# Performance work log

Hardware: AMD Instinct MI355X
Metric: run time of the kernel (lower is better)

Reference implementation:

```python
import jax, jax.numpy as jnp
import numpy as np

H2 = 512  # 2 * hidden_dim
B, TK = 64, 2048


def setup_inputs() -> dict:
    key = jax.random.key(0)
    ks = jax.random.split(key, 10)
    s_t_hat = jax.random.normal(ks[0], (B, H2), dtype=jnp.float32)
    encoder_outputs = jax.random.normal(ks[1], (B, TK, H2), dtype=jnp.float32)
    encoder_feature = jax.random.normal(ks[2], (B, TK, H2), dtype=jnp.float32)
    enc_padding_mask = jnp.ones((B, TK), dtype=jnp.float32)
    coverage = jax.random.uniform(ks[3], (B, TK), dtype=jnp.float32)
    # learned params (torch Linear stores W as [out, in]; we keep math explicit)
    sc = 1.0 / np.sqrt(H2)
    W_dp = jax.random.uniform(ks[4], (H2, H2), minval=-sc, maxval=sc, dtype=jnp.float32)  # decode_proj weight [out,in]
    b_dp = jax.random.uniform(ks[5], (H2,), minval=-sc, maxval=sc, dtype=jnp.float32)
    W_c = jax.random.uniform(ks[6], (H2,), minval=-1.0, maxval=1.0, dtype=jnp.float32)  # Linear(1, 2H) weight, squeezed
    v_w = jax.random.uniform(ks[7], (H2,), minval=-sc, maxval=sc, dtype=jnp.float32)  # Linear(2H, 1) weight
    v_b = jax.random.uniform(ks[8], (), minval=-sc, maxval=sc, dtype=jnp.float32)
    return {
        "s_t_hat": s_t_hat,
        "encoder_outputs": encoder_outputs,
        "encoder_feature": encoder_feature,
        "enc_padding_mask": enc_padding_mask,
        "coverage": coverage,
        "W_dp": W_dp,
        "b_dp": b_dp,
        "W_c": W_c,
        "v_w": v_w,
        "v_b": v_b,
    }


def reference(s_t_hat, encoder_outputs, encoder_feature, enc_padding_mask, coverage,
              W_dp, b_dp, W_c, v_w, v_b):
    # decoder projection: [b, n]
    dec_fea = s_t_hat @ W_dp.T + b_dp
    # broadcast add over t_k, plus coverage feature (Linear(1, 2H) == outer product)
    att_features = encoder_feature + dec_fea[:, None, :] + coverage[:, :, None] * W_c  # [b, t_k, n]
    e = jnp.tanh(att_features)
    scores = jnp.einsum('btn,n->bt', e, v_w) + v_b  # [b, t_k]
    attn_ = jax.nn.softmax(scores, axis=1) * enc_padding_mask
    attn = attn_ / jnp.sum(attn_, axis=1, keepdims=True)  # renormalized [b, t_k]
    c_t = jnp.einsum('bt,btn->bn', attn, encoder_outputs)  # [b, n]
    coverage_new = coverage + attn
    return (c_t, attn, coverage_new)
```

## Files before the change

### kernel.cpp

```cpp
#include <hip/hip_runtime.h>
#include <math.h>

#define H2 512
#define NB 64
#define TK 2048
#define SPLIT 16

#define LOG2E 1.44269504088896f
#define TWO_LOG2E 2.88539008177793f

__global__ __launch_bounds__(256) void k_decproj(const float* __restrict__ s,
                                                 const float* __restrict__ W,
                                                 const float* __restrict__ bias,
                                                 float* __restrict__ dec) {
    const int bb = blockIdx.x;
    const int wave = threadIdx.x >> 6;
    const int lane = threadIdx.x & 63;
    const float* srow = s + bb * H2;
    float4 s0 = *(const float4*)(srow + lane * 8);
    float4 s1 = *(const float4*)(srow + lane * 8 + 4);
    #pragma unroll
    for (int i = 0; i < 8; ++i) {
        const int n = blockIdx.y * 32 + wave * 8 + i;
        const float* wrow = W + (size_t)n * H2;
        float4 w0 = *(const float4*)(wrow + lane * 8);
        float4 w1 = *(const float4*)(wrow + lane * 8 + 4);
        float acc = s0.x * w0.x + s0.y * w0.y + s0.z * w0.z + s0.w * w0.w +
                    s1.x * w1.x + s1.y * w1.y + s1.z * w1.z + s1.w * w1.w;
        #pragma unroll
        for (int off = 1; off < 64; off <<= 1) acc += __shfl_xor(acc, off, 64);
        if (lane == 0) dec[bb * H2 + n] = acc + bias[n];
    }
}

template <int REP>
__global__ __launch_bounds__(256) void k_scores2(const float* __restrict__ ef,
                                                 const float* __restrict__ cov,
                                                 const float* __restrict__ mask,
                                                 const float* __restrict__ dec,
                                                 const float* __restrict__ wc,
                                                 const float* __restrict__ vw,
                                                 const float* __restrict__ vbp,
                                                 float* __restrict__ w) {
    const int bb = blockIdx.y;
    const int t0 = blockIdx.x * 64;
    const int tid = threadIdx.x;
    const int wave = tid >> 6, lane = tid & 63;
    const int n0 = lane * 8;

    __shared__ float pl[64][68];

    float4 d0 = *(const float4*)(dec + bb * H2 + n0);
    float4 d1 = *(const float4*)(dec + bb * H2 + n0 + 4);
    float4 c0 = *(const float4*)(wc + n0);
    float4 c1 = *(const float4*)(wc + n0 + 4);
    float4 v0 = *(const float4*)(vw + n0);
    float4 v1 = *(const float4*)(vw + n0 + 4);

    float vwsum = v0.x + v0.y + v0.z + v0.w + v1.x + v1.y + v1.z + v1.w;
    #pragma unroll
    for (int off = 1; off < 64; off <<= 1) vwsum += __shfl_xor(vwsum, off, 64);

    d0.x *= TWO_LOG2E; d0.y *= TWO_LOG2E; d0.z *= TWO_LOG2E; d0.w *= TWO_LOG2E;
    d1.x *= TWO_LOG2E; d1.y *= TWO_LOG2E; d1.z *= TWO_LOG2E; d1.w *= TWO_LOG2E;
    c0.x *= TWO_LOG2E; c0.y *= TWO_LOG2E; c0.z *= TWO_LOG2E; c0.w *= TWO_LOG2E;
    c1.x *= TWO_LOG2E; c1.y *= TWO_LOG2E; c1.z *= TWO_LOG2E; c1.w *= TWO_LOG2E;
    v0.x *= -2.f; v0.y *= -2.f; v0.z *= -2.f; v0.w *= -2.f;
    v1.x *= -2.f; v1.y *= -2.f; v1.z *= -2.f; v1.w *= -2.f;
    const float vb = vbp[0];

    const size_t rowbase = (size_t)bb * TK + t0;

    #pragma unroll 1
    for (int rep = 0; rep < REP; ++rep) {
        float4 ea[2][4][2];
        float cv[2][4];
        #pragma unroll
        for (int i = 0; i < 4; ++i) {
            const int r = wave + 4 * i;
            const float* p = ef + (rowbase + r) * H2 + n0;
            ea[0][i][0] = *(const float4*)p;
            ea[0][i][1] = *(const float4*)(p + 4);
            cv[0][i] = cov[rowbase + r];
        }
        #pragma unroll
        for (int j0 = 0; j0 < 16; j0 += 4) {
            const int cur = (j0 >> 2) & 1;
            const int nxt = cur ^ 1;
            if (j0 + 4 < 16) {
                #pragma unroll
                for (int i = 0; i < 4; ++i) {
                    const int r = wave + 4 * (j0 + 4 + i);
                    const float* p = ef + (rowbase + r) * H2 + n0;
                    ea[nxt][i][0] = *(const float4*)p;
                    ea[nxt][i][1] = *(const float4*)(p + 4);
                    cv[nxt][i] = cov[rowbase + r];
                }
            }
            #pragma unroll
            for (int i = 0; i < 4; ++i) {
                const float cvv = cv[cur][i];
                #define TERM(E, D, C, V) \
                    ((V) * __builtin_amdgcn_rcpf(__builtin_amdgcn_exp2f(fmaf((E), TWO_LOG2E, fmaf(cvv, (C), (D)))) + 1.0f))
                const float acc =
                    TERM(ea[cur][i][0].x, d0.x, c0.x, v0.x) + TERM(ea[cur][i][0].y, d0.y, c0.y, v0.y) +
                    TERM(ea[cur][i][0].z, d0.z, c0.z, v0.z) + TERM(ea[cur][i][0].w, d0.w, c0.w, v0.w) +
                    TERM(ea[cur][i][1].x, d1.x, c1.x, v1.x) + TERM(ea[cur][i][1].y, d1.y, c1.y, v1.y) +
                    TERM(ea[cur][i][1].z, d1.z, c1.z, v1.z) + TERM(ea[cur][i][1].w, d1.w, c1.w, v1.w);
                #undef TERM
                pl[wave + 4 * (j0 + i)][lane] = acc;
            }
        }
        __syncthreads();

        const int r = tid >> 2, q = tid & 3;
        const float* prow = &pl[r][q * 16];
        const float4 x0 = *(const float4*)(prow);
        const float4 x1 = *(const float4*)(prow + 4);
        const float4 x2 = *(const float4*)(prow + 8);
        const float4 x3 = *(const float4*)(prow + 12);
        float s = x0.x + x0.y + x0.z + x0.w + x1.x + x1.y + x1.z + x1.w +
                  x2.x + x2.y + x2.z + x2.w + x3.x + x3.y + x3.z + x3.w;
        s += __shfl_xor(s, 1, 64);
        s += __shfl_xor(s, 2, 64);
        if (q == 0) {
            const float score = vwsum + s + vb;
            w[rowbase + r] = __builtin_amdgcn_exp2f(score * LOG2E) * mask[rowbase + r];
        }
        __syncthreads();
    }
}

template <int REP>
__global__ __launch_bounds__(256) void k_ctpart(const float* __restrict__ eo,
                                                const float* __restrict__ w,
                                                float* __restrict__ part) {
    const int bb = blockIdx.y, sp = blockIdx.x;
    const int tid = threadIdx.x;
    const int ng = tid & 127, th = tid >> 7;
    const int t0 = sp * 128 + th * 64;
    const float* wp = w + bb * TK + t0;
    const float4* ep = (const float4*)(eo + ((size_t)bb * TK + t0) * H2) + ng;
    __shared__ float4 red[128];

    #define FMA4(a, r) do { acc.x = fmaf((a), (r).x, acc.x); acc.y = fmaf((a), (r).y, acc.y); \
                            acc.z = fmaf((a), (r).z, acc.z); acc.w = fmaf((a), (r).w, acc.w); } while (0)

    #pragma unroll 1
    for (int rep = 0; rep < REP; ++rep) {
        float4 acc = make_float4(0.f, 0.f, 0.f, 0.f);
        float4 rr[2][8];
        float4 wv[2][2];
        #pragma unroll
        for (int i = 0; i < 8; ++i) rr[0][i] = ep[(size_t)i * 128];
        wv[0][0] = *(const float4*)(wp);
        wv[0][1] = *(const float4*)(wp + 4);

        #pragma unroll
        for (int c = 0; c < 8; ++c) {
            const int cur = c & 1, nxt = cur ^ 1;
            if (c < 7) {
                const int base = (c + 1) * 8;
                #pragma unroll
                for (int i = 0; i < 8; ++i) rr[nxt][i] = ep[(size_t)(base + i) * 128];
                wv[nxt][0] = *(const float4*)(wp + base);
                wv[nxt][1] = *(const float4*)(wp + base + 4);
            }
            FMA4(wv[cur][0].x, rr[cur][0]);
            FMA4(wv[cur][0].y, rr[cur][1]);
            FMA4(wv[cur][0].z, rr[cur][2]);
            FMA4(wv[cur][0].w, rr[cur][3]);
            FMA4(wv[cur][1].x, rr[cur][4]);
            FMA4(wv[cur][1].y, rr[cur][5]);
            FMA4(wv[cur][1].z, rr[cur][6]);
            FMA4(wv[cur][1].w, rr[cur][7]);
        }

        if (th) red[ng] = acc;
        __syncthreads();
        if (!th) {
            const float4 o = red[ng];
            acc.x += o.x; acc.y += o.y; acc.z += o.z; acc.w += o.w;
            *(float4*)(part + ((size_t)bb * SPLIT + sp) * H2 + ng * 4) = acc;
        }
        __syncthreads();
    }
    #undef FMA4
}

__global__ __launch_bounds__(512) void k_finish(const float* __restrict__ w,
                                                const float* __restrict__ cov,
                                                const float* __restrict__ part,
                                                float* __restrict__ attn,
                                                float* __restrict__ covnew,
                                                float* __restrict__ ct) {
    const int bb = blockIdx.x;
    const int tid = threadIdx.x;
    const int lane = tid & 63, wave = tid >> 6;

    const float4 w4 = *(const float4*)(w + bb * TK + tid * 4);
    float s = w4.x + w4.y + w4.z + w4.w;
    #pragma unroll
    for (int off = 1; off < 64; off <<= 1) s += __shfl_xor(s, off, 64);
    __shared__ float rs[8];
    if (lane == 0) rs[wave] = s;
    __syncthreads();
    s = rs[0] + rs[1] + rs[2] + rs[3] + rs[4] + rs[5] + rs[6] + rs[7];
    const float inv = 1.0f / s;

    const float4 c4 = *(const float4*)(cov + bb * TK + tid * 4);
    float4 a4, n4;
    a4.x = w4.x * inv; a4.y = w4.y * inv; a4.z = w4.z * inv; a4.w = w4.w * inv;
    n4.x = c4.x + a4.x; n4.y = c4.y + a4.y; n4.z = c4.z + a4.z; n4.w = c4.w + a4.w;
    *(float4*)(attn + bb * TK + tid * 4) = a4;
    *(float4*)(covnew + bb * TK + tid * 4) = n4;

    float acc = 0.f;
    #pragma unroll
    for (int sp = 0; sp < SPLIT; ++sp) acc += part[((size_t)bb * SPLIT + sp) * H2 + tid];
    ct[bb * H2 + tid] = acc * inv;
}

extern "C" void kernel_launch(void* const* d_in, const int* in_sizes, int n_in,
                              void* d_out, int out_size, void* d_ws, size_t ws_size,
                              hipStream_t stream) {
    const float* s_t_hat  = (const float*)d_in[0];
    const float* enc_out  = (const float*)d_in[1];
    const float* enc_feat = (const float*)d_in[2];
    const float* mask     = (const float*)d_in[3];
    const float* cov      = (const float*)d_in[4];
    const float* W_dp     = (const float*)d_in[5];
    const float* b_dp     = (const float*)d_in[6];
    const float* W_c      = (const float*)d_in[7];
    const float* v_w      = (const float*)d_in[8];
    const float* v_b      = (const float*)d_in[9];

    float* out = (float*)d_out;
    float* ct     = out;
    float* attn   = out + NB * H2;
    float* covnew = attn + NB * TK;

    float* dec  = (float*)d_ws;
    float* w    = dec + NB * H2;
    float* part = w + NB * TK;

    k_decproj<<<dim3(NB, 16), 256, 0, stream>>>(s_t_hat, W_dp, b_dp, dec);
    k_scores2<4><<<dim3(TK / 64, NB), 256, 0, stream>>>(enc_feat, cov, mask, dec, W_c, v_w, v_b, w);
    k_ctpart<4><<<dim3(SPLIT, NB), 256, 0, stream>>>(enc_out, w, part);
    k_finish<<<NB, 512, 0, stream>>>(w, cov, part, attn, covnew, ct);
}
```

Measured before the change: 113.6 us.

## Fuse score and context-partial kernels into one tile-level kernel

Merges the score kernel and the context partial-sum kernel so each block computes unnormalized attention weights for a 64-row tile, keeps them in LDS, then immediately accumulates the weighted encoder_outputs rows into a per-tile partial. This drops one kernel launch and the global round trip of the weights between stages, and lets the encoder_outputs streaming of one block overlap with the tanh compute of others. The grid shrinks to 32x64 blocks with no REP loop, and the finish kernel now reduces 32 partials per batch instead of 16.

Measured after the change: 109.5 us, median of 2. -3.6%, faster.

```diff
diff --git a/kernel.cpp b/kernel.cpp
--- a/kernel.cpp
+++ b/kernel.cpp
@@ -4,7 +4,7 @@
 #define H2 512
 #define NB 64
 #define TK 2048
-#define SPLIT 16
+#define NTILE 32
 
 #define LOG2E 1.44269504088896f
 #define TWO_LOG2E 2.88539008177793f
@@ -33,22 +33,26 @@
     }
 }
 
-template <int REP>
-__global__ __launch_bounds__(256) void k_scores2(const float* __restrict__ ef,
-                                                 const float* __restrict__ cov,
-                                                 const float* __restrict__ mask,
-                                                 const float* __restrict__ dec,
-                                                 const float* __restrict__ wc,
-                                                 const float* __restrict__ vw,
-                                                 const float* __restrict__ vbp,
-                                                 float* __restrict__ w) {
+__global__ __launch_bounds__(256) void k_fused2(const float* __restrict__ ef,
+                                                const float* __restrict__ eo,
+                                                const float* __restrict__ cov,
+                                                const float* __restrict__ mask,
+                                                const float* __restrict__ dec,
+                                                const float* __restrict__ wc,
+                                                const float* __restrict__ vw,
+                                                const float* __restrict__ vbp,
+                                                float* __restrict__ w,
+                                                float* __restrict__ part) {
     const int bb = blockIdx.y;
-    const int t0 = blockIdx.x * 64;
+    const int tile = blockIdx.x;
+    const int t0 = tile * 64;
     const int tid = threadIdx.x;
     const int wave = tid >> 6, lane = tid & 63;
     const int n0 = lane * 8;
 
     __shared__ float pl[64][68];
+    __shared__ float e_lds[64];
+    float4* const red = (float4*)&pl[0][0];
 
     float4 d0 = *(const float4*)(dec + bb * H2 + n0);
     float4 d1 = *(const float4*)(dec + bb * H2 + n0 + 4);
@@ -71,8 +75,7 @@
 
     const size_t rowbase = (size_t)bb * TK + t0;
 
-    #pragma unroll 1
-    for (int rep = 0; rep < REP; ++rep) {
+    {
         float4 ea[2][4][2];
         float cv[2][4];
         #pragma unroll
@@ -111,8 +114,10 @@
                 pl[wave + 4 * (j0 + i)][lane] = acc;
             }
         }
-        __syncthreads();
-
+    }
+    __syncthreads();
+
+    {
         const int r = tid >> 2, q = tid & 3;
         const float* prow = &pl[r][q * 16];
         const float4 x0 = *(const float4*)(prow);
@@ -125,75 +130,56 @@
         s += __shfl_xor(s, 2, 64);
         if (q == 0) {
             const float score = vwsum + s + vb;
-            w[rowbase + r] = __builtin_amdgcn_exp2f(score * LOG2E) * mask[rowbase + r];
-        }
-        __syncthreads();
-    }
-}
-
-template <int REP>
-__global__ __launch_bounds__(256) void k_ctpart(const float* __restrict__ eo,
-                                                const float* __restrict__ w,
-                                                float* __restrict__ part) {
-    const int bb = blockIdx.y, sp = blockIdx.x;
-    const int tid = threadIdx.x;
+            const float e = __builtin_amdgcn_exp2f(score * LOG2E) * mask[rowbase + r];
+            e_lds[r] = e;
+            w[rowbase + r] = e;
+        }
+    }
+    __syncthreads();
+
     const int ng = tid & 127, th = tid >> 7;
-    const int t0 = sp * 128 + th * 64;
-    const float* wp = w + bb * TK + t0;
-    const float4* ep = (const float4*)(eo + ((size_t)bb * TK + t0) * H2) + ng;
-    __shared__ float4 red[128];
+    const int rb = th * 32;
+    const float4* ep = (const float4*)(eo + (rowbase + rb) * H2) + ng;
 
     #define FMA4(a, r) do { acc.x = fmaf((a), (r).x, acc.x); acc.y = fmaf((a), (r).y, acc.y); \
                             acc.z = fmaf((a), (r).z, acc.z); acc.w = fmaf((a), (r).w, acc.w); } while (0)
-
-    #pragma unroll 1
-    for (int rep = 0; rep < REP; ++rep) {
-        float4 acc = make_float4(0.f, 0.f, 0.f, 0.f);
-        float4 rr[2][8];
-        float4 wv[2][2];
-        #pragma unroll
-        for (int i = 0; i < 8; ++i) rr[0][i] = ep[(size_t)i * 128];
-        wv[0][0] = *(const float4*)(wp);
-        wv[0][1] = *(const float4*)(wp + 4);
-
-        #pragma unroll
-        for (int c = 0; c < 8; ++c) {
-            const int cur = c & 1, nxt = cur ^ 1;
-            if (c < 7) {
-                const int base = (c + 1) * 8;
-                #pragma unroll
-                for (int i = 0; i < 8; ++i) rr[nxt][i] = ep[(size_t)(base + i) * 128];
-                wv[nxt][0] = *(const float4*)(wp + base);
-                wv[nxt][1] = *(const float4*)(wp + base + 4);
+    float4 acc = make_float4(0.f, 0.f, 0.f, 0.f);
+    float4 rr[2][8];
+    float we[2][8];
+    #pragma unroll
+    for (int i = 0; i < 8; ++i) { rr[0][i] = ep[(size_t)i * 128]; we[0][i] = e_lds[rb + i]; }
+
+    #pragma unroll
+    for (int c = 0; c < 4; ++c) {
+        const int cur = c & 1, nxt = cur ^ 1;
+        if (c < 3) {
+            const int base = (c + 1) * 8;
+            #pragma unroll
+            for (int i = 0; i < 8; ++i) {
+                rr[nxt][i] = ep[(size_t)(base + i) * 128];
+                we[nxt][i] = e_lds[rb + base + i];
             }
-            FMA4(wv[cur][0].x, rr[cur][0]);
-            FMA4(wv[cur][0].y, rr[cur][1]);
-            FMA4(wv[cur][0].z, rr[cur][2]);
-            FMA4(wv[cur][0].w, rr[cur][3]);
-            FMA4(wv[cur][1].x, rr[cur][4]);
-            FMA4(wv[cur][1].y, rr[cur][5]);
-            FMA4(wv[cur][1].z, rr[cur][6]);
-            FMA4(wv[cur][1].w, rr[cur][7]);
-        }
-
-        if (th) red[ng] = acc;
-        __syncthreads();
-        if (!th) {
-            const float4 o = red[ng];
-            acc.x += o.x; acc.y += o.y; acc.z += o.z; acc.w += o.w;
-            *(float4*)(part + ((size_t)bb * SPLIT + sp) * H2 + ng * 4) = acc;
-        }
-        __syncthreads();
+        }
+        #pragma unroll
+        for (int i = 0; i < 8; ++i) FMA4(we[cur][i], rr[cur][i]);
     }
     #undef FMA4
-}
-
-__global__ __launch_bounds__(512) void k_finish(const float* __restrict__ w,
-                                                const float* __restrict__ cov,
-                                                const float* __restrict__ part,
-                                                float* __restrict__ attn,
-                                                float* __restrict__ covnew,
-                                                float* __restrict__ ct) {
+
+    if (th) red[ng] = acc;
+    __syncthreads();
+    if (!th) {
+        const float4 o = red[ng];
+        acc.x += o.x; acc.y += o.y; acc.z += o.z; acc.w += o.w;
+        *(float4*)(part + ((size_t)bb * NTILE + tile) * H2 + ng * 4) = acc;
+    }
+}
+
+__global__ __launch_bounds__(512) void k_finish2(const float* __restrict__ w,
+                                                 const float* __restrict__ cov,
+                                                 const float* __restrict__ part,
+                                                 float* __restrict__ attn,
+                                                 float* __restrict__ covnew,
+                                                 float* __restrict__ ct) {
     const int bb = blockIdx.x;
     const int tid = threadIdx.x;
     const int lane = tid & 63, wave = tid >> 6;
@@ -217,7 +203,7 @@
 
     float acc = 0.f;
     #pragma unroll
-    for (int sp = 0; sp < SPLIT; ++sp) acc += part[((size_t)bb * SPLIT + sp) * H2 + tid];
+    for (int t = 0; t < NTILE; ++t) acc += part[((size_t)bb * NTILE + t) * H2 + tid];
     ct[bb * H2 + tid] = acc * inv;
 }
 
@@ -245,7 +231,7 @@
     float* part = w + NB * TK;
 
     k_decproj<<<dim3(NB, 16), 256, 0, stream>>>(s_t_hat, W_dp, b_dp, dec);
-    k_scores2<4><<<dim3(TK / 64, NB), 256, 0, stream>>>(enc_feat, cov, mask, dec, W_c, v_w, v_b, w);
-    k_ctpart<4><<<dim3(SPLIT, NB), 256, 0, stream>>>(enc_out, w, part);
-    k_finish<<<NB, 512, 0, stream>>>(w, cov, part, attn, covnew, ct);
-}
+    k_fused2<<<dim3(NTILE, NB), 256, 0, stream>>>(enc_feat, enc_out, cov, mask, dec,
+                                                  W_c, v_w, v_b, w, part);
+    k_finish2<<<NB, 512, 0, stream>>>(w, cov, part, attn, covnew, ct);
+}
```
